# Optimization experiments

Measured on AMD Instinct MI355X. Metric: run time of the kernel, lower is better.

## Reference

```python
import jax, jax.numpy as jnp
import numpy as np

S = 32768      # number of time points
DIM = 64       # system dimension
H = 16         # n_harmonics (fixed; original draws randint(2,20))


def setup_inputs() -> dict:
    key = jax.random.key(0)
    ks = jax.random.split(key, 7)
    s = jax.random.uniform(ks[0], (S,), dtype=jnp.float32)          # time points
    x = jax.random.normal(ks[1], (S, DIM), dtype=jnp.float32)       # unused by forward, kept for signature
    A = jax.random.uniform(ks[2], (DIM, H, 2), dtype=jnp.float32, minval=-10.0, maxval=10.0)
    phi = jax.random.uniform(ks[3], (DIM, H, 2), dtype=jnp.float32, minval=-1.0, maxval=1.0)
    w = jax.random.uniform(ks[4], (DIM, H, 2), dtype=jnp.float32, minval=-20.0, maxval=20.0)
    bound = 1.0 / np.sqrt(DIM)
    W = jax.random.uniform(ks[5], (DIM, DIM), dtype=jnp.float32, minval=-bound, maxval=bound)
    b = jax.random.uniform(ks[6], (DIM,), dtype=jnp.float32, minval=-bound, maxval=bound)
    return {"s": s, "x": x, "A": A, "phi": phi, "w": w, "W": W, "b": b}


def reference(s, x, A, phi, w, W, b):
    # Vectorized over all time points and both cosine components at once.
    # phases: [S, dim, H, 2]
    phases = w[None] * s[:, None, None, None] + phi[None]
    pre_sol = jnp.sum(A[None] * jnp.cos(phases), axis=(2, 3))  # [S, dim]
    return pre_sol @ W.T + b  # Linear(dim, dim)
```

## Files before the change

### kernel.cpp

```cpp
#include <hip/hip_runtime.h>


typedef float    f32x2 __attribute__((ext_vector_type(2)));
typedef float    f32x4 __attribute__((ext_vector_type(4)));
typedef _Float16 f16x8 __attribute__((ext_vector_type(8)));

constexpr int S_PTS = 32768;
constexpr int DIM   = 64;
constexpr int HC    = 32;
constexpr int TPW   = 16;
constexpr float INV_2PI = 0.15915494309189535f;

static __device__ __forceinline__ unsigned pkrtz(float x, float y) {
    return __builtin_bit_cast(unsigned, __builtin_amdgcn_cvt_pkrtz(x, y));
}
static __device__ __forceinline__ f16x8 pack8(float4 a, float4 b) {
    union { unsigned u[4]; f16x8 v; } t;
    t.u[0] = pkrtz(a.x, a.y);
    t.u[1] = pkrtz(a.z, a.w);
    t.u[2] = pkrtz(b.x, b.y);
    t.u[3] = pkrtz(b.z, b.w);
    return t.v;
}

__global__ __launch_bounds__(256, 2)
void fourier_fused(const float* __restrict__ s,
                   const float* __restrict__ A,
                   const float* __restrict__ phi,
                   const float* __restrict__ w,
                   const float* __restrict__ Wm,
                   const float* __restrict__ b,
                   float* __restrict__ out)
{
    __shared__ float slab[4][TPW * DIM];

    const int lane = threadIdx.x & 63;
    const int wid  = threadIdx.x >> 6;
    const int t0   = (blockIdx.x * 4 + wid) * TPW;
    const int t16  = lane & 15;
    const int hi   = lane >> 4;

    f32x2 a2[16], w2[16], p2[16];
    {
        const float4* A4 = reinterpret_cast<const float4*>(A   + lane * HC);
        const float4* P4 = reinterpret_cast<const float4*>(phi + lane * HC);
        const float4* W4 = reinterpret_cast<const float4*>(w   + lane * HC);
        #pragma unroll
        for (int q = 0; q < 8; ++q) {
            float4 av = A4[q], pv = P4[q], wv = W4[q];
            a2[2*q+0] = f32x2{av.x, av.y};           a2[2*q+1] = f32x2{av.z, av.w};
            p2[2*q+0] = f32x2{pv.x, pv.y} * INV_2PI; p2[2*q+1] = f32x2{pv.z, pv.w} * INV_2PI;
            w2[2*q+0] = f32x2{wv.x, wv.y} * INV_2PI; w2[2*q+1] = f32x2{wv.z, wv.w} * INV_2PI;
        }
    }

    f16x8 wf[4][2];
    float bj[4];
    #pragma unroll
    for (int n = 0; n < 4; ++n) {
        const float* wr = Wm + (n * 16 + t16) * DIM;
        #pragma unroll
        for (int ks = 0; ks < 2; ++ks) {
            float4 v0 = *reinterpret_cast<const float4*>(wr + ks * 32 + hi * 8);
            float4 v1 = *reinterpret_cast<const float4*>(wr + ks * 32 + hi * 8 + 4);
            wf[n][ks] = pack8(v0, v1);
        }
        bj[n] = b[n * 16 + t16];
    }

    const float sv = s[t0 + t16];
    float* myslab = slab[wid];

    #pragma unroll
    for (int k = 0; k < TPW; ++k) {
        const float st = __uint_as_float(__builtin_amdgcn_readlane(__float_as_uint(sv), k));
        const f32x2 st2 = {st, st};
        f32x2 ac0 = {0.f, 0.f}, ac1 = {0.f, 0.f};
        #pragma unroll
        for (int i = 0; i < 16; i += 2) {
            f32x2 ph0 = w2[i+0] * st2 + p2[i+0];
            f32x2 ph1 = w2[i+1] * st2 + p2[i+1];
            f32x2 c0 = { __builtin_amdgcn_cosf(ph0[0]), __builtin_amdgcn_cosf(ph0[1]) };
            f32x2 c1 = { __builtin_amdgcn_cosf(ph1[0]), __builtin_amdgcn_cosf(ph1[1]) };
            ac0 = a2[i+0] * c0 + ac0;
            ac1 = a2[i+1] * c1 + ac1;
        }
        const f32x2 acs = ac0 + ac1;
        myslab[(k * 64 + lane) ^ ((k & 7) << 2)] = acs[0] + acs[1];
    }
    asm volatile("s_waitcnt lgkmcnt(0)" ::: "memory");

    f16x8 pa[2];
    #pragma unroll
    for (int ks = 0; ks < 2; ++ks) {
        const int base = t16 * 64 + ks * 32 + hi * 8;
        const int w0 = base       ^ ((t16 & 7) << 2);
        const int w1 = (base + 4) ^ ((t16 & 7) << 2);
        float4 q0 = *reinterpret_cast<const float4*>(myslab + w0);
        float4 q1 = *reinterpret_cast<const float4*>(myslab + w1);
        pa[ks] = pack8(q0, q1);
    }

    f32x4 acc0 = {}, acc1 = {}, acc2 = {}, acc3 = {};
    acc0 = __builtin_amdgcn_mfma_f32_16x16x32_f16(pa[0], wf[0][0], acc0, 0, 0, 0);
    acc0 = __builtin_amdgcn_mfma_f32_16x16x32_f16(pa[1], wf[0][1], acc0, 0, 0, 0);
    acc1 = __builtin_amdgcn_mfma_f32_16x16x32_f16(pa[0], wf[1][0], acc1, 0, 0, 0);
    acc1 = __builtin_amdgcn_mfma_f32_16x16x32_f16(pa[1], wf[1][1], acc1, 0, 0, 0);
    acc2 = __builtin_amdgcn_mfma_f32_16x16x32_f16(pa[0], wf[2][0], acc2, 0, 0, 0);
    acc2 = __builtin_amdgcn_mfma_f32_16x16x32_f16(pa[1], wf[2][1], acc2, 0, 0, 0);
    acc3 = __builtin_amdgcn_mfma_f32_16x16x32_f16(pa[0], wf[3][0], acc3, 0, 0, 0);
    acc3 = __builtin_amdgcn_mfma_f32_16x16x32_f16(pa[1], wf[3][1], acc3, 0, 0, 0);

    #pragma unroll
    for (int r = 0; r < 4; ++r) {
        const int trow = (t0 + hi * 4 + r) * DIM;
        out[trow +  0 + t16] = acc0[r] + bj[0];
        out[trow + 16 + t16] = acc1[r] + bj[1];
        out[trow + 32 + t16] = acc2[r] + bj[2];
        out[trow + 48 + t16] = acc3[r] + bj[3];
    }
}

extern "C" void kernel_launch(void* const* d_in, const int* in_sizes, int n_in,
                              void* d_out, int out_size, void* d_ws, size_t ws_size,
                              hipStream_t stream) {
    const float* s   = (const float*)d_in[0];
    const float* A   = (const float*)d_in[2];
    const float* phi = (const float*)d_in[3];
    const float* w   = (const float*)d_in[4];
    const float* Wm  = (const float*)d_in[5];
    const float* b   = (const float*)d_in[6];
    float* out = (float*)d_out;

    dim3 grid(S_PTS / (4 * TPW));
    dim3 block(256);
    hipLaunchKernelGGL(fourier_fused, grid, block, 0, stream,
                       s, A, phi, w, Wm, b, out);
}
```

Measured before the change: 17.48 us.

## Split harmonic sum across wave pairs and halve per-wave MFMA output columns

Each time tile is now handled by a pair of waves. Each wave computes half of the harmonic terms into its own LDS slab, and after a block barrier both partial sums are added when loading the MFMA A fragments. Each wave then computes only half of the output columns. This halves register arrays per wave and raises the launch-bounds occupancy hint from 2 to 4, doubling the grid to expose more parallelism, at the cost of a __syncthreads and extra LDS reads.

```diff
diff --git a/kernel.cpp b/kernel.cpp
--- a/kernel.cpp
+++ b/kernel.cpp
@@ -8,22 +8,22 @@
 constexpr int S_PTS = 32768;
 constexpr int DIM   = 64;
 constexpr int HC    = 32;
-constexpr int TPW   = 16;
+constexpr int TPP   = 16;
 constexpr float INV_2PI = 0.15915494309189535f;
 
 static __device__ __forceinline__ unsigned pkrtz(float x, float y) {
     return __builtin_bit_cast(unsigned, __builtin_amdgcn_cvt_pkrtz(x, y));
 }
-static __device__ __forceinline__ f16x8 pack8(float4 a, float4 b) {
+static __device__ __forceinline__ f16x8 pack8(f32x4 a, f32x4 b) {
     union { unsigned u[4]; f16x8 v; } t;
-    t.u[0] = pkrtz(a.x, a.y);
-    t.u[1] = pkrtz(a.z, a.w);
-    t.u[2] = pkrtz(b.x, b.y);
-    t.u[3] = pkrtz(b.z, b.w);
+    t.u[0] = pkrtz(a[0], a[1]);
+    t.u[1] = pkrtz(a[2], a[3]);
+    t.u[2] = pkrtz(b[0], b[1]);
+    t.u[3] = pkrtz(b[2], b[3]);
     return t.v;
 }
 
-__global__ __launch_bounds__(256, 2)
+__global__ __launch_bounds__(256, 4)
 void fourier_fused(const float* __restrict__ s,
                    const float* __restrict__ A,
                    const float* __restrict__ phi,
@@ -32,21 +32,23 @@
                    const float* __restrict__ b,
                    float* __restrict__ out)
 {
-    __shared__ float slab[4][TPW * DIM];
+    __shared__ float pf[2][2][TPP * DIM];
 
     const int lane = threadIdx.x & 63;
     const int wid  = threadIdx.x >> 6;
-    const int t0   = (blockIdx.x * 4 + wid) * TPW;
+    const int pair = wid >> 1;
+    const int half = wid & 1;
+    const int t0   = blockIdx.x * (2 * TPP) + pair * TPP;
     const int t16  = lane & 15;
     const int hi   = lane >> 4;
 
-    f32x2 a2[16], w2[16], p2[16];
+    f32x2 a2[8], w2[8], p2[8];
     {
-        const float4* A4 = reinterpret_cast<const float4*>(A   + lane * HC);
-        const float4* P4 = reinterpret_cast<const float4*>(phi + lane * HC);
-        const float4* W4 = reinterpret_cast<const float4*>(w   + lane * HC);
+        const float4* A4 = reinterpret_cast<const float4*>(A   + lane * HC + half * 16);
+        const float4* P4 = reinterpret_cast<const float4*>(phi + lane * HC + half * 16);
+        const float4* W4 = reinterpret_cast<const float4*>(w   + lane * HC + half * 16);
         #pragma unroll
-        for (int q = 0; q < 8; ++q) {
+        for (int q = 0; q < 4; ++q) {
             float4 av = A4[q], pv = P4[q], wv = W4[q];
             a2[2*q+0] = f32x2{av.x, av.y};           a2[2*q+1] = f32x2{av.z, av.w};
             p2[2*q+0] = f32x2{pv.x, pv.y} * INV_2PI; p2[2*q+1] = f32x2{pv.z, pv.w} * INV_2PI;
@@ -54,30 +56,31 @@
         }
     }
 
-    f16x8 wf[4][2];
-    float bj[4];
+    f16x8 wf[2][2];
+    float bj[2];
     #pragma unroll
-    for (int n = 0; n < 4; ++n) {
+    for (int nn = 0; nn < 2; ++nn) {
+        const int n = half * 2 + nn;
         const float* wr = Wm + (n * 16 + t16) * DIM;
         #pragma unroll
         for (int ks = 0; ks < 2; ++ks) {
-            float4 v0 = *reinterpret_cast<const float4*>(wr + ks * 32 + hi * 8);
-            float4 v1 = *reinterpret_cast<const float4*>(wr + ks * 32 + hi * 8 + 4);
-            wf[n][ks] = pack8(v0, v1);
+            f32x4 v0 = *reinterpret_cast<const f32x4*>(wr + ks * 32 + hi * 8);
+            f32x4 v1 = *reinterpret_cast<const f32x4*>(wr + ks * 32 + hi * 8 + 4);
+            wf[nn][ks] = pack8(v0, v1);
         }
-        bj[n] = b[n * 16 + t16];
+        bj[nn] = b[n * 16 + t16];
     }
 
     const float sv = s[t0 + t16];
-    float* myslab = slab[wid];
+    float* myslab = pf[pair][half];
 
     #pragma unroll
-    for (int k = 0; k < TPW; ++k) {
+    for (int k = 0; k < TPP; ++k) {
         const float st = __uint_as_float(__builtin_amdgcn_readlane(__float_as_uint(sv), k));
         const f32x2 st2 = {st, st};
         f32x2 ac0 = {0.f, 0.f}, ac1 = {0.f, 0.f};
         #pragma unroll
-        for (int i = 0; i < 16; i += 2) {
+        for (int i = 0; i < 8; i += 2) {
             f32x2 ph0 = w2[i+0] * st2 + p2[i+0];
             f32x2 ph1 = w2[i+1] * st2 + p2[i+1];
             f32x2 c0 = { __builtin_amdgcn_cosf(ph0[0]), __builtin_amdgcn_cosf(ph0[1]) };
@@ -88,36 +91,35 @@
         const f32x2 acs = ac0 + ac1;
         myslab[(k * 64 + lane) ^ ((k & 7) << 2)] = acs[0] + acs[1];
     }
-    asm volatile("s_waitcnt lgkmcnt(0)" ::: "memory");
+    __syncthreads();
 
+    const float* s0 = pf[pair][0];
+    const float* s1 = pf[pair][1];
     f16x8 pa[2];
     #pragma unroll
     for (int ks = 0; ks < 2; ++ks) {
         const int base = t16 * 64 + ks * 32 + hi * 8;
         const int w0 = base       ^ ((t16 & 7) << 2);
         const int w1 = (base + 4) ^ ((t16 & 7) << 2);
-        float4 q0 = *reinterpret_cast<const float4*>(myslab + w0);
-        float4 q1 = *reinterpret_cast<const float4*>(myslab + w1);
+        f32x4 q0 = *reinterpret_cast<const f32x4*>(s0 + w0)
+                 + *reinterpret_cast<const f32x4*>(s1 + w0);
+        f32x4 q1 = *reinterpret_cast<const f32x4*>(s0 + w1)
+                 + *reinterpret_cast<const f32x4*>(s1 + w1);
         pa[ks] = pack8(q0, q1);
     }
 
-    f32x4 acc0 = {}, acc1 = {}, acc2 = {}, acc3 = {};
+    f32x4 acc0 = {}, acc1 = {};
     acc0 = __builtin_amdgcn_mfma_f32_16x16x32_f16(pa[0], wf[0][0], acc0, 0, 0, 0);
     acc0 = __builtin_amdgcn_mfma_f32_16x16x32_f16(pa[1], wf[0][1], acc0, 0, 0, 0);
     acc1 = __builtin_amdgcn_mfma_f32_16x16x32_f16(pa[0], wf[1][0], acc1, 0, 0, 0);
     acc1 = __builtin_amdgcn_mfma_f32_16x16x32_f16(pa[1], wf[1][1], acc1, 0, 0, 0);
-    acc2 = __builtin_amdgcn_mfma_f32_16x16x32_f16(pa[0], wf[2][0], acc2, 0, 0, 0);
-    acc2 = __builtin_amdgcn_mfma_f32_16x16x32_f16(pa[1], wf[2][1], acc2, 0, 0, 0);
-    acc3 = __builtin_amdgcn_mfma_f32_16x16x32_f16(pa[0], wf[3][0], acc3, 0, 0, 0);
-    acc3 = __builtin_amdgcn_mfma_f32_16x16x32_f16(pa[1], wf[3][1], acc3, 0, 0, 0);
 
+    const int c0 = half * 32 + t16;
     #pragma unroll
     for (int r = 0; r < 4; ++r) {
         const int trow = (t0 + hi * 4 + r) * DIM;
-        out[trow +  0 + t16] = acc0[r] + bj[0];
-        out[trow + 16 + t16] = acc1[r] + bj[1];
-        out[trow + 32 + t16] = acc2[r] + bj[2];
-        out[trow + 48 + t16] = acc3[r] + bj[3];
+        out[trow + c0 +  0] = acc0[r] + bj[0];
+        out[trow + c0 + 16] = acc1[r] + bj[1];
     }
 }
 
@@ -132,7 +134,7 @@
     const float* b   = (const float*)d_in[6];
     float* out = (float*)d_out;
 
-    dim3 grid(S_PTS / (4 * TPW));
+    dim3 grid(S_PTS / (2 * TPP));
     dim3 block(256);
     hipLaunchKernelGGL(fourier_fused, grid, block, 0, stream,
                        s, A, phi, w, Wm, b, out);
```

Result: slower. 19.03 us (+8.9%).
